# Kernel optimization log

Hardware: AMD Instinct MI355X
Metric: run time of the kernel (lower is better)

The kernel has to match this reference:

```python
import jax, jax.numpy as jnp
import numpy as np

D_MODEL = 2048
N_HEADS = 16
HEAD_DIM = D_MODEL // N_HEADS  # 128
BASE = 10000.0
NEG = -1e9


def _rope_tables(seq_len, dtype=jnp.float32):
    # inv_freq over even dims of head_dim, emb = cat(freqs, freqs)
    inv_freq = 1.0 / (BASE ** (jnp.arange(0, HEAD_DIM, 2, dtype=jnp.float32) / HEAD_DIM))
    t = jnp.arange(seq_len, dtype=jnp.float32)
    freqs = jnp.einsum('i,j->ij', t, inv_freq)          # [S, hd/2]
    emb = jnp.concatenate([freqs, freqs], axis=-1)       # [S, hd]
    return jnp.cos(emb).astype(dtype)[None, None], jnp.sin(emb).astype(dtype)[None, None]


def _rotate_half(x):
    # Faithful to source: rotary_ndims == head_dim, so x2 is empty and this returns x.
    x1, x2 = x[..., :HEAD_DIM], x[..., HEAD_DIM:]
    return jnp.concatenate([-x2, x1], axis=-1)


def setup_inputs() -> dict:
    key = jax.random.key(0)
    ks = jax.random.split(key, 5)
    B, S = 2, 2048
    x = jax.random.normal(ks[0], (B, S, D_MODEL), dtype=jnp.float32)
    # additive causal mask [1,1,S,S]
    causal = jnp.tril(jnp.ones((S, S), dtype=bool))
    attention_mask = jnp.where(causal, 0.0, NEG).astype(jnp.float32)[None, None]
    scale = 1.0 / np.sqrt(D_MODEL)
    Wq = jax.random.normal(ks[1], (D_MODEL, D_MODEL), dtype=jnp.float32) * scale
    Wk = jax.random.normal(ks[2], (D_MODEL, D_MODEL), dtype=jnp.float32) * scale
    Wv = jax.random.normal(ks[3], (D_MODEL, D_MODEL), dtype=jnp.float32) * scale
    Wd = jax.random.normal(ks[4], (D_MODEL, D_MODEL), dtype=jnp.float32) * scale
    return {"x": x, "attention_mask": attention_mask, "Wq": Wq, "Wk": Wk, "Wv": Wv, "Wd": Wd}


def reference(x, attention_mask, Wq, Wk, Wv, Wd):
    B, S, _ = x.shape
    # torch Linear: y = x @ W.T  (weights stored [out, in])
    def proj(W):
        y = jnp.einsum('bsd,ed->bse', x, W)
        return y.reshape(B, S, N_HEADS, HEAD_DIM).transpose(0, 2, 1, 3)  # [B,H,S,hd]
    q, k, v = proj(Wq), proj(Wk), proj(Wv)
    cos, sin = _rope_tables(S, x.dtype)
    q = q * cos + _rotate_half(q) * sin
    k = k * cos + _rotate_half(k) * sin
    scores = jnp.einsum('bhqd,bhkd->bhqk', q, k) / jnp.sqrt(jnp.float32(HEAD_DIM)).astype(x.dtype)
    scores = scores + attention_mask
    attn = jax.nn.softmax(scores, axis=-1)
    out = jnp.einsum('bhqk,bhkd->bhqd', attn, v)
    out = out.transpose(0, 2, 1, 3).reshape(B, S, D_MODEL)
    return jnp.einsum('bse,de->bsd', out, Wd)
```

## Files before the change

kernel.cpp:

```cpp
#include <hip/hip_runtime.h>
#include <stdint.h>

#define DM   2048
#define NH   16
#define HD   128
#define BB   2
#define SS   2048
#define MM   (BB*SS)
#define KK   2048
#define NQKV (3*DM)

#define LOG2E  1.4426950408889634f
#define SCALE  0.08838834764831845f

using bf16x8 = __attribute__((ext_vector_type(8))) __bf16;
using f32x4  = __attribute__((ext_vector_type(4))) float;
typedef unsigned short u16;
typedef unsigned int   u32;

__device__ __forceinline__ u16 f2bf(float f) {
  u32 u = __float_as_uint(f);
  u32 r = (u + 0x7FFFu + ((u >> 16) & 1u)) >> 16;
  return (u16)r;
}

__device__ __forceinline__ void load_lds16(const void* g, void* l) {
  __builtin_amdgcn_global_load_lds(
      (__attribute__((address_space(1))) void*)(g),
      (__attribute__((address_space(3))) void*)(l), 16, 0, 0);
}

__global__ void cast_f32_bf16(const float* __restrict__ s, u16* __restrict__ d, int n) {
  int i = (blockIdx.x * blockDim.x + threadIdx.x) * 4;
  if (i < n) {
    float4 f = *(const float4*)(s + i);
    u32 lo = (u32)f2bf(f.x) | ((u32)f2bf(f.y) << 16);
    u32 hi = (u32)f2bf(f.z) | ((u32)f2bf(f.w) << 16);
    *(uint2*)(d + i) = make_uint2(lo, hi);
  }
}

__global__ void rope_fct(float* __restrict__ f) {
  int i = blockIdx.x * blockDim.x + threadIdx.x;
  if (i < SS * 128) {
    int s = i >> 7, j = i & 127;
    double inv = pow(10000.0, -(double)(j & 63) / 64.0);
    float ang = (float)s * (float)inv;
    float sn, cs;
    sincosf(ang, &sn, &cs);
    f[i] = cs + sn;
  }
}

__global__ __launch_bounds__(256, 2)
void gemm_qkv_rope(const u16* __restrict__ A, const u16* __restrict__ Bm,
                   u16* __restrict__ qo, u16* __restrict__ ko, u16* __restrict__ vo,
                   const float* __restrict__ fct) {
  __shared__ __align__(16) u16 S[2][128 * 32];
  u16* As = S[0];
  u16* Bs = S[1];
  const int tid = threadIdx.x;
  const int w = tid >> 6, lane = tid & 63, ln = lane & 15, quad = lane >> 4;
  const int m0 = blockIdx.x * 128, n0 = blockIdx.y * 128;

  const f32x4 fz = {0.f, 0.f, 0.f, 0.f};
  f32x4 acc[2][8];
#pragma unroll
  for (int mt = 0; mt < 2; mt++)
#pragma unroll
    for (int nt = 0; nt < 8; nt++) acc[mt][nt] = fz;

  for (int k0 = 0; k0 < KK; k0 += 32) {
    __syncthreads();
#pragma unroll
    for (int i = 0; i < 2; i++) {
      int tt = i * 256 + tid;
      load_lds16(A + (size_t)(m0 + (tt >> 2)) * KK + k0 + (tt & 3) * 8, (char*)As + tt * 16);
    }
#pragma unroll
    for (int i = 0; i < 2; i++) {
      int tt = i * 256 + tid;
      load_lds16(Bm + (size_t)(n0 + (tt >> 2)) * KK + k0 + (tt & 3) * 8, (char*)Bs + tt * 16);
    }
    __syncthreads();
    bf16x8 af[2];
#pragma unroll
    for (int mt = 0; mt < 2; mt++)
      af[mt] = *(const bf16x8*)&As[(w * 32 + mt * 16 + ln) * 32 + quad * 8];
#pragma unroll
    for (int nt = 0; nt < 8; nt++) {
      bf16x8 bf = *(const bf16x8*)&Bs[(nt * 16 + ln) * 32 + quad * 8];
#pragma unroll
      for (int mt = 0; mt < 2; mt++)
        acc[mt][nt] = __builtin_amdgcn_mfma_f32_16x16x32_bf16(af[mt], bf, acc[mt][nt], 0, 0, 0);
    }
  }

  const int tensor = n0 >> 11;
  const int h = (n0 & 2047) >> 7;
  if (tensor < 2) {
    u16* dst = (tensor == 0) ? qo : ko;
#pragma unroll
    for (int mt = 0; mt < 2; mt++)
#pragma unroll
      for (int r = 0; r < 4; r++) {
        int m = m0 + w * 32 + mt * 16 + quad * 4 + r;
        int b = m >> 11, s = m & 2047;
        size_t base = ((size_t)(b * NH + h) * SS + s) * HD;
        const float* fr = fct + s * 128;
#pragma unroll
        for (int nt = 0; nt < 8; nt++) {
          int j = nt * 16 + ln;
          dst[base + j] = f2bf(acc[mt][nt][r] * fr[j]);
        }
      }
  } else {
    u16* Tr = (u16*)S;
    const int b = m0 >> 11, s0 = m0 & 2047;
#pragma unroll
    for (int mt = 0; mt < 2; mt++) {
      __syncthreads();
#pragma unroll
      for (int nt = 0; nt < 8; nt++) {
        int hd = nt * 16 + ln;
#pragma unroll
        for (int r = 0; r < 4; r++) {
          int c = w * 16 + quad * 4 + r;
          Tr[hd * 64 + (((c >> 3) ^ (hd & 7)) * 8) + (c & 7)] = f2bf(acc[mt][nt][r]);
        }
      }
      __syncthreads();
#pragma unroll
      for (int it = 0; it < 4; it++) {
        int idx = it * 256 + tid;
        int hd = idx >> 3, c8 = idx & 7;
        uint4 val = *(const uint4*)&Tr[hd * 64 + ((c8 ^ (hd & 7)) * 8)];
        int c0 = c8 * 8;
        int srel = ((c0 >> 4) * 32) + mt * 16 + (c0 & 15);
        *(uint4*)(vo + ((size_t)(b * NH + h) * HD + hd) * SS + s0 + srel) = val;
      }
    }
  }
}

__global__ __launch_bounds__(256, 2)
void flash_attn(const u16* __restrict__ q, const u16* __restrict__ k,
                const u16* __restrict__ v, u16* __restrict__ o) {
  __shared__ __align__(16) u16 Ps[64 * 64];
  __shared__ __align__(16) u16 Ks[2][64 * 128];
  __shared__ __align__(16) u16 Vs[2][128 * 64];
  const int tid = threadIdx.x;
  const int w = tid >> 6, lane = tid & 63, ln = lane & 15, quad = lane >> 4;
  const int hh = blockIdx.y, b = blockIdx.z;
  const size_t bh = (size_t)b * NH + hh;
  const u16* Kg = k + bh * SS * HD;
  const u16* Vg = v + bh * HD * SS;

  for (int half = 0; half < 2; half++) {
    const int T = half ? (31 - (int)blockIdx.x) : (int)blockIdx.x;
    const u16* Qg = q + bh * SS * HD + (size_t)T * 64 * HD;

    bf16x8 qf[4];
#pragma unroll
    for (int kc = 0; kc < 4; kc++)
      qf[kc] = *(const bf16x8*)(Qg + (size_t)(w * 16 + ln) * HD + (kc * 4 + quad) * 8);

    __syncthreads();

#pragma unroll
    for (int i = 0; i < 4; i++) {
      int slot = i * 256 + tid;
      int r = slot >> 4, c = (slot & 15) ^ (r & 7);
      load_lds16(Kg + (size_t)r * HD + c * 8, (char*)Ks[0] + slot * 16);
    }
#pragma unroll
    for (int i = 0; i < 4; i++) {
      int slot = i * 256 + tid;
      int r = slot >> 3, c = (slot & 7) ^ (r & 7);
      load_lds16(Vg + (size_t)r * SS + c * 8, (char*)Vs[0] + slot * 16);
    }

    const f32x4 fz = {0.f, 0.f, 0.f, 0.f};
    float m_s[4], l_s[4];
    f32x4 accO[8];
#pragma unroll
    for (int r = 0; r < 4; r++) { m_s[r] = -1e30f; l_s[r] = 0.f; }
#pragma unroll
    for (int nt = 0; nt < 8; nt++) accO[nt] = fz;

    const int nkt = T + 1;
    const int qrb = T * 64 + w * 16;

    for (int kt = 0; kt < nkt; kt++) {
      const int cur = kt & 1;
      const int k0 = kt * 64;
      __asm__ __volatile__("s_waitcnt vmcnt(0)" ::: "memory");
      __syncthreads();
      if (kt + 1 < nkt) {
        const int kn = k0 + 64;
#pragma unroll
        for (int i = 0; i < 4; i++) {
          int slot = i * 256 + tid;
          int r = slot >> 4, c = (slot & 15) ^ (r & 7);
          load_lds16(Kg + (size_t)(kn + r) * HD + c * 8, (char*)Ks[cur ^ 1] + slot * 16);
        }
#pragma unroll
        for (int i = 0; i < 4; i++) {
          int slot = i * 256 + tid;
          int r = slot >> 3, c = (slot & 7) ^ (r & 7);
          load_lds16(Vg + (size_t)r * SS + kn + c * 8, (char*)Vs[cur ^ 1] + slot * 16);
        }
      }

      f32x4 sc[4];
#pragma unroll
      for (int nt = 0; nt < 4; nt++) sc[nt] = fz;
#pragma unroll
      for (int kc = 0; kc < 4; kc++)
#pragma unroll
        for (int nt = 0; nt < 4; nt++) {
          bf16x8 bf = *(const bf16x8*)&Ks[cur][(nt * 16 + ln) * 128 + (((kc * 4 + quad) ^ (ln & 7)) * 8)];
          sc[nt] = __builtin_amdgcn_mfma_f32_16x16x32_bf16(qf[kc], bf, sc[nt], 0, 0, 0);
        }

      const bool partial = (kt == T);
#pragma unroll
      for (int nt = 0; nt < 4; nt++)
#pragma unroll
        for (int r = 0; r < 4; r++) {
          float val = sc[nt][r] * SCALE;
          if (partial && (k0 + nt * 16 + ln > qrb + quad * 4 + r)) val = -1e9f;
          sc[nt][r] = val;
        }

#pragma unroll
      for (int r = 0; r < 4; r++) {
        float mx = fmaxf(fmaxf(sc[0][r], sc[1][r]), fmaxf(sc[2][r], sc[3][r]));
#pragma unroll
        for (int off = 1; off < 16; off <<= 1) mx = fmaxf(mx, __shfl_xor(mx, off));
        float mnew = fmaxf(m_s[r], mx);
        float alpha = exp2f((m_s[r] - mnew) * LOG2E);
        float rs = 0.f;
#pragma unroll
        for (int nt = 0; nt < 4; nt++) {
          float p = exp2f((sc[nt][r] - mnew) * LOG2E);
          sc[nt][r] = p;
          rs += p;
        }
#pragma unroll
        for (int off = 1; off < 16; off <<= 1) rs += __shfl_xor(rs, off);
        l_s[r] = l_s[r] * alpha + rs;
        m_s[r] = mnew;
#pragma unroll
        for (int nt = 0; nt < 8; nt++) accO[nt][r] *= alpha;
      }

#pragma unroll
      for (int nt = 0; nt < 4; nt++)
#pragma unroll
        for (int r = 0; r < 4; r++) {
          int rr = w * 16 + quad * 4 + r;
          int j = nt * 16 + ln;
          Ps[rr * 64 + (((j >> 3) ^ (rr & 7)) * 8) + (j & 7)] = f2bf(sc[nt][r]);
        }
      __asm__ __volatile__("s_waitcnt lgkmcnt(0)" ::: "memory");

      bf16x8 pf[2];
#pragma unroll
      for (int kc = 0; kc < 2; kc++) {
        int rp = w * 16 + ln;
        pf[kc] = *(const bf16x8*)&Ps[rp * 64 + (((kc * 4 + quad) ^ (ln & 7)) * 8)];
      }

#pragma unroll
      for (int kc = 0; kc < 2; kc++)
#pragma unroll
        for (int nt = 0; nt < 8; nt++) {
          bf16x8 vf = *(const bf16x8*)&Vs[cur][(nt * 16 + ln) * 64 + (((kc * 4 + quad) ^ (ln & 7)) * 8)];
          accO[nt] = __builtin_amdgcn_mfma_f32_16x16x32_bf16(pf[kc], vf, accO[nt], 0, 0, 0);
        }
    }

#pragma unroll
    for (int r = 0; r < 4; r++) {
      float ilv = 1.f / l_s[r];
      int srow = T * 64 + w * 16 + quad * 4 + r;
      size_t base = ((size_t)b * SS + srow) * DM + hh * HD;
#pragma unroll
      for (int nt = 0; nt < 8; nt++)
        o[base + nt * 16 + ln] = f2bf(accO[nt][r] * ilv);
    }
  }
}

__global__ __launch_bounds__(256, 2)
void gemm_out(const u16* __restrict__ A, const u16* __restrict__ Bm,
              float* __restrict__ C) {
  __shared__ __align__(16) u16 As[128 * 32];
  __shared__ __align__(16) u16 Bs[128 * 32];
  const int tid = threadIdx.x;
  const int w = tid >> 6, lane = tid & 63, ln = lane & 15, quad = lane >> 4;
  const int m0 = blockIdx.x * 128, n0 = blockIdx.y * 128;

  const f32x4 fz = {0.f, 0.f, 0.f, 0.f};
  f32x4 acc[2][8];
#pragma unroll
  for (int mt = 0; mt < 2; mt++)
#pragma unroll
    for (int nt = 0; nt < 8; nt++) acc[mt][nt] = fz;

  for (int k0 = 0; k0 < KK; k0 += 32) {
    __syncthreads();
#pragma unroll
    for (int i = 0; i < 2; i++) {
      int tt = i * 256 + tid;
      load_lds16(A + (size_t)(m0 + (tt >> 2)) * KK + k0 + (tt & 3) * 8, (char*)As + tt * 16);
    }
#pragma unroll
    for (int i = 0; i < 2; i++) {
      int tt = i * 256 + tid;
      load_lds16(Bm + (size_t)(n0 + (tt >> 2)) * KK + k0 + (tt & 3) * 8, (char*)Bs + tt * 16);
    }
    __syncthreads();
    bf16x8 af[2];
#pragma unroll
    for (int mt = 0; mt < 2; mt++)
      af[mt] = *(const bf16x8*)&As[(w * 32 + mt * 16 + ln) * 32 + quad * 8];
#pragma unroll
    for (int nt = 0; nt < 8; nt++) {
      bf16x8 bf = *(const bf16x8*)&Bs[(nt * 16 + ln) * 32 + quad * 8];
#pragma unroll
      for (int mt = 0; mt < 2; mt++)
        acc[mt][nt] = __builtin_amdgcn_mfma_f32_16x16x32_bf16(af[mt], bf, acc[mt][nt], 0, 0, 0);
    }
  }

#pragma unroll
  for (int mt = 0; mt < 2; mt++)
#pragma unroll
    for (int r = 0; r < 4; r++) {
      int m = m0 + w * 32 + mt * 16 + quad * 4 + r;
#pragma unroll
      for (int nt = 0; nt < 8; nt++)
        C[(size_t)m * DM + n0 + nt * 16 + ln] = acc[mt][nt][r];
    }
}

extern "C" void kernel_launch(void* const* d_in, const int* in_sizes, int n_in,
                              void* d_out, int out_size, void* d_ws, size_t ws_size,
                              hipStream_t stream) {
  (void)in_sizes; (void)n_in; (void)out_size; (void)ws_size;
  const float* x  = (const float*)d_in[0];
  const float* Wq = (const float*)d_in[2];
  const float* Wk = (const float*)d_in[3];
  const float* Wv = (const float*)d_in[4];
  const float* Wd = (const float*)d_in[5];

  char* ws = (char*)d_ws;
  u16* xb   = (u16*)(ws);
  u16* aob  = xb;
  u16* wqkv = (u16*)(ws + 16777216ull);
  float* fct = (float*)(ws + 41943040ull);
  u16* wdb  = (u16*)(ws + 41943040ull);
  u16* qb   = (u16*)(ws + 50331648ull);
  u16* kb   = (u16*)(ws + 67108864ull);
  u16* vtb  = (u16*)(ws + 83886080ull);

  cast_f32_bf16<<<8192, 256, 0, stream>>>(x,  xb, MM * KK);
  cast_f32_bf16<<<4096, 256, 0, stream>>>(Wq, wqkv,                   DM * KK);
  cast_f32_bf16<<<4096, 256, 0, stream>>>(Wk, wqkv + (size_t)DM*KK,   DM * KK);
  cast_f32_bf16<<<4096, 256, 0, stream>>>(Wv, wqkv + (size_t)2*DM*KK, DM * KK);
  rope_fct<<<1024, 256, 0, stream>>>(fct);

  gemm_qkv_rope<<<dim3(MM / 128, NQKV / 128), 256, 0, stream>>>(xb, wqkv, qb, kb, vtb, fct);

  cast_f32_bf16<<<4096, 256, 0, stream>>>(Wd, wdb, DM * KK);

  flash_attn<<<dim3(16, NH, BB), 256, 0, stream>>>(qb, kb, vtb, aob);
  gemm_out<<<dim3(MM / 128, DM / 128), 256, 0, stream>>>(aob, wdb, (float*)d_out);
}
```

Measured before the change: 423.2 us.

## Rewrite QKV GEMM with 256x256 tiles, double-buffered LDS and interleaved async loads

The QKV projection GEMM moves from 128x128 tiles with 256 threads and a synchronous k-step of 32 to 256x256 tiles with 512 threads and a k-step of 64. It uses XOR-swizzled, double-buffered LDS and stages the next tile in quarters between MFMA phases, with manual waitcnt, barrier and setprio control. The goal is more data reuse per load and hiding global-load latency behind MFMA work. In exchange it uses 128KB of LDS and a large accumulator set, which likely limits occupancy to one block per CU despite the launch bounds, and the V transpose epilogue is rewritten to match.

```diff
diff --git a/kernel.cpp b/kernel.cpp
--- a/kernel.cpp
+++ b/kernel.cpp
@@ -52,93 +52,195 @@
   }
 }
 
-__global__ __launch_bounds__(256, 2)
+
+__device__ __forceinline__ void stage_half(const u16* __restrict__ G, int rowbase,
+                                           int kbase, int h, u16* lds, int tid) {
+#pragma unroll
+  for (int i = 0; i < 2; i++) {
+    int s = i * 512 + tid;
+    int r = s >> 3, c = s & 7;
+    load_lds16(G + (size_t)(rowbase + h * 128 + r) * KK + kbase + ((c ^ (r & 7)) * 8),
+               (char*)lds + (size_t)(h * 1024 + s) * 16);
+  }
+}
+
+__global__ __launch_bounds__(512, 2)
 void gemm_qkv_rope(const u16* __restrict__ A, const u16* __restrict__ Bm,
                    u16* __restrict__ qo, u16* __restrict__ ko, u16* __restrict__ vo,
                    const float* __restrict__ fct) {
-  __shared__ __align__(16) u16 S[2][128 * 32];
-  u16* As = S[0];
-  u16* Bs = S[1];
+  __shared__ __align__(16) u16 L[2][2][256 * 64];
   const int tid = threadIdx.x;
-  const int w = tid >> 6, lane = tid & 63, ln = lane & 15, quad = lane >> 4;
-  const int m0 = blockIdx.x * 128, n0 = blockIdx.y * 128;
+  const int wid = tid >> 6, lane = tid & 63, ln = lane & 15, quad = lane >> 4;
+  const int wm = wid >> 2, wn = wid & 3;
+  const int m0 = blockIdx.x * 256, n0 = blockIdx.y * 256;
 
   const f32x4 fz = {0.f, 0.f, 0.f, 0.f};
-  f32x4 acc[2][8];
-#pragma unroll
-  for (int mt = 0; mt < 2; mt++)
-#pragma unroll
-    for (int nt = 0; nt < 8; nt++) acc[mt][nt] = fz;
-
-  for (int k0 = 0; k0 < KK; k0 += 32) {
-    __syncthreads();
-#pragma unroll
-    for (int i = 0; i < 2; i++) {
-      int tt = i * 256 + tid;
-      load_lds16(A + (size_t)(m0 + (tt >> 2)) * KK + k0 + (tt & 3) * 8, (char*)As + tt * 16);
-    }
-#pragma unroll
-    for (int i = 0; i < 2; i++) {
-      int tt = i * 256 + tid;
-      load_lds16(Bm + (size_t)(n0 + (tt >> 2)) * KK + k0 + (tt & 3) * 8, (char*)Bs + tt * 16);
-    }
-    __syncthreads();
-    bf16x8 af[2];
-#pragma unroll
-    for (int mt = 0; mt < 2; mt++)
-      af[mt] = *(const bf16x8*)&As[(w * 32 + mt * 16 + ln) * 32 + quad * 8];
-#pragma unroll
-    for (int nt = 0; nt < 8; nt++) {
-      bf16x8 bf = *(const bf16x8*)&Bs[(nt * 16 + ln) * 32 + quad * 8];
-#pragma unroll
-      for (int mt = 0; mt < 2; mt++)
-        acc[mt][nt] = __builtin_amdgcn_mfma_f32_16x16x32_bf16(af[mt], bf, acc[mt][nt], 0, 0, 0);
-    }
+  f32x4 acc[8][4];
+#pragma unroll
+  for (int mi = 0; mi < 8; mi++)
+#pragma unroll
+    for (int ni = 0; ni < 4; ni++) acc[mi][ni] = fz;
+
+  int aRow[8], bRow[4];
+#pragma unroll
+  for (int mi = 0; mi < 8; mi++)
+    aRow[mi] = ((mi < 4) ? (wm * 64 + mi * 16) : (128 + wm * 64 + (mi - 4) * 16)) + ln;
+#pragma unroll
+  for (int ni = 0; ni < 4; ni++)
+    bRow[ni] = ((ni < 2) ? (wn * 32 + ni * 16) : (128 + wn * 32 + (ni - 2) * 16)) + ln;
+
+  stage_half(A,  m0, 0, 0, L[0][0], tid);
+  stage_half(Bm, n0, 0, 0, L[0][1], tid);
+  stage_half(A,  m0, 0, 1, L[0][0], tid);
+  stage_half(Bm, n0, 0, 1, L[0][1], tid);
+
+  const int nT = KK / 64;
+  for (int t = 0; t < nT; t++) {
+    const int cur = t & 1;
+    const u16* At = L[cur][0];
+    const u16* Bt = L[cur][1];
+    u16* Ax = L[cur ^ 1][0];
+    u16* Bx = L[cur ^ 1][1];
+    const int kn = (t + 1) * 64;
+    const bool nl = (t + 1 < nT);
+    bf16x8 aF[2][4], bF0[2][2], bF1[2][2];
+
+    if (nl) { __asm__ __volatile__("s_waitcnt vmcnt(4)" ::: "memory"); }
+    else    { __asm__ __volatile__("s_waitcnt vmcnt(0)" ::: "memory"); }
+    __asm__ __volatile__("s_barrier" ::: "memory");
+#pragma unroll
+    for (int kk = 0; kk < 2; kk++) {
+#pragma unroll
+      for (int mi = 0; mi < 4; mi++)
+        aF[kk][mi] = *(const bf16x8*)&At[aRow[mi] * 64 + (((kk * 4 + quad) ^ (aRow[mi] & 7)) * 8)];
+#pragma unroll
+      for (int ni = 0; ni < 2; ni++)
+        bF0[kk][ni] = *(const bf16x8*)&Bt[bRow[ni] * 64 + (((kk * 4 + quad) ^ (bRow[ni] & 7)) * 8)];
+    }
+    if (nl) stage_half(A, m0, kn, 0, Ax, tid);
+    __asm__ __volatile__("s_waitcnt lgkmcnt(0)" ::: "memory");
+    __builtin_amdgcn_sched_barrier(0);
+    __builtin_amdgcn_s_setprio(1);
+#pragma unroll
+    for (int kk = 0; kk < 2; kk++)
+#pragma unroll
+      for (int mi = 0; mi < 4; mi++)
+#pragma unroll
+        for (int ni = 0; ni < 2; ni++)
+          acc[mi][ni] = __builtin_amdgcn_mfma_f32_16x16x32_bf16(aF[kk][mi], bF0[kk][ni], acc[mi][ni], 0, 0, 0);
+    __builtin_amdgcn_s_setprio(0);
+    __builtin_amdgcn_sched_barrier(0);
+
+    if (nl) { __asm__ __volatile__("s_waitcnt vmcnt(4)" ::: "memory"); }
+    __asm__ __volatile__("s_barrier" ::: "memory");
+#pragma unroll
+    for (int kk = 0; kk < 2; kk++)
+#pragma unroll
+      for (int mi = 0; mi < 4; mi++)
+        aF[kk][mi] = *(const bf16x8*)&At[aRow[4 + mi] * 64 + (((kk * 4 + quad) ^ (aRow[4 + mi] & 7)) * 8)];
+    if (nl) stage_half(Bm, n0, kn, 0, Bx, tid);
+    __asm__ __volatile__("s_waitcnt lgkmcnt(0)" ::: "memory");
+    __builtin_amdgcn_sched_barrier(0);
+    __builtin_amdgcn_s_setprio(1);
+#pragma unroll
+    for (int kk = 0; kk < 2; kk++)
+#pragma unroll
+      for (int mi = 0; mi < 4; mi++)
+#pragma unroll
+        for (int ni = 0; ni < 2; ni++)
+          acc[4 + mi][ni] = __builtin_amdgcn_mfma_f32_16x16x32_bf16(aF[kk][mi], bF0[kk][ni], acc[4 + mi][ni], 0, 0, 0);
+    __builtin_amdgcn_s_setprio(0);
+    __builtin_amdgcn_sched_barrier(0);
+
+    if (nl) { __asm__ __volatile__("s_waitcnt vmcnt(4)" ::: "memory"); }
+    __asm__ __volatile__("s_barrier" ::: "memory");
+#pragma unroll
+    for (int kk = 0; kk < 2; kk++)
+#pragma unroll
+      for (int ni = 0; ni < 2; ni++)
+        bF1[kk][ni] = *(const bf16x8*)&Bt[bRow[2 + ni] * 64 + (((kk * 4 + quad) ^ (bRow[2 + ni] & 7)) * 8)];
+    if (nl) stage_half(A, m0, kn, 1, Ax, tid);
+    __asm__ __volatile__("s_waitcnt lgkmcnt(0)" ::: "memory");
+    __builtin_amdgcn_sched_barrier(0);
+    __builtin_amdgcn_s_setprio(1);
+#pragma unroll
+    for (int kk = 0; kk < 2; kk++)
+#pragma unroll
+      for (int mi = 0; mi < 4; mi++)
+#pragma unroll
+        for (int ni = 0; ni < 2; ni++)
+          acc[4 + mi][2 + ni] = __builtin_amdgcn_mfma_f32_16x16x32_bf16(aF[kk][mi], bF1[kk][ni], acc[4 + mi][2 + ni], 0, 0, 0);
+    __builtin_amdgcn_s_setprio(0);
+    __builtin_amdgcn_sched_barrier(0);
+
+#pragma unroll
+    for (int kk = 0; kk < 2; kk++)
+#pragma unroll
+      for (int mi = 0; mi < 4; mi++)
+        aF[kk][mi] = *(const bf16x8*)&At[aRow[mi] * 64 + (((kk * 4 + quad) ^ (aRow[mi] & 7)) * 8)];
+    if (nl) stage_half(Bm, n0, kn, 1, Bx, tid);
+    __asm__ __volatile__("s_waitcnt lgkmcnt(0)" ::: "memory");
+    __builtin_amdgcn_sched_barrier(0);
+    __builtin_amdgcn_s_setprio(1);
+#pragma unroll
+    for (int kk = 0; kk < 2; kk++)
+#pragma unroll
+      for (int mi = 0; mi < 4; mi++)
+#pragma unroll
+        for (int ni = 0; ni < 2; ni++)
+          acc[mi][2 + ni] = __builtin_amdgcn_mfma_f32_16x16x32_bf16(aF[kk][mi], bF1[kk][ni], acc[mi][2 + ni], 0, 0, 0);
+    __builtin_amdgcn_s_setprio(0);
+    __builtin_amdgcn_sched_barrier(0);
   }
 
   const int tensor = n0 >> 11;
-  const int h = (n0 & 2047) >> 7;
+  const int nloc0 = n0 & 2047;
   if (tensor < 2) {
     u16* dst = (tensor == 0) ? qo : ko;
 #pragma unroll
-    for (int mt = 0; mt < 2; mt++)
+    for (int mi = 0; mi < 8; mi++) {
+      int rowM = (mi < 4) ? (wm * 64 + mi * 16) : (128 + wm * 64 + (mi - 4) * 16);
 #pragma unroll
       for (int r = 0; r < 4; r++) {
-        int m = m0 + w * 32 + mt * 16 + quad * 4 + r;
+        int m = m0 + rowM + quad * 4 + r;
         int b = m >> 11, s = m & 2047;
-        size_t base = ((size_t)(b * NH + h) * SS + s) * HD;
         const float* fr = fct + s * 128;
 #pragma unroll
-        for (int nt = 0; nt < 8; nt++) {
-          int j = nt * 16 + ln;
-          dst[base + j] = f2bf(acc[mt][nt][r] * fr[j]);
+        for (int ni = 0; ni < 4; ni++) {
+          int colN = ((ni < 2) ? (wn * 32 + ni * 16) : (128 + wn * 32 + (ni - 2) * 16)) + ln;
+          int h = (nloc0 + colN) >> 7;
+          int j = colN & 127;
+          dst[((size_t)(b * NH + h) * SS + s) * HD + j] = f2bf(acc[mi][ni][r] * fr[j]);
         }
       }
+    }
   } else {
-    u16* Tr = (u16*)S;
+    __syncthreads();
+    u16* Tr = (u16*)L;
     const int b = m0 >> 11, s0 = m0 & 2047;
 #pragma unroll
-    for (int mt = 0; mt < 2; mt++) {
-      __syncthreads();
-#pragma unroll
-      for (int nt = 0; nt < 8; nt++) {
-        int hd = nt * 16 + ln;
+    for (int mi = 0; mi < 8; mi++) {
+      int rowM = (mi < 4) ? (wm * 64 + mi * 16) : (128 + wm * 64 + (mi - 4) * 16);
+#pragma unroll
+      for (int ni = 0; ni < 4; ni++) {
+        int colN = ((ni < 2) ? (wn * 32 + ni * 16) : (128 + wn * 32 + (ni - 2) * 16)) + ln;
 #pragma unroll
         for (int r = 0; r < 4; r++) {
-          int c = w * 16 + quad * 4 + r;
-          Tr[hd * 64 + (((c >> 3) ^ (hd & 7)) * 8) + (c & 7)] = f2bf(acc[mt][nt][r]);
+          int srel = rowM + quad * 4 + r;
+          int ch = srel >> 3;
+          Tr[colN * 256 + ((ch ^ (colN & 31)) * 8) + (srel & 7)] = f2bf(acc[mi][ni][r]);
         }
       }
-      __syncthreads();
-#pragma unroll
-      for (int it = 0; it < 4; it++) {
-        int idx = it * 256 + tid;
-        int hd = idx >> 3, c8 = idx & 7;
-        uint4 val = *(const uint4*)&Tr[hd * 64 + ((c8 ^ (hd & 7)) * 8)];
-        int c0 = c8 * 8;
-        int srel = ((c0 >> 4) * 32) + mt * 16 + (c0 & 15);
-        *(uint4*)(vo + ((size_t)(b * NH + h) * HD + hd) * SS + s0 + srel) = val;
-      }
+    }
+    __syncthreads();
+#pragma unroll
+    for (int it = 0; it < 16; it++) {
+      int slot = it * 512 + tid;
+      int nloc = slot >> 5, c8 = slot & 31;
+      uint4 val = *(const uint4*)&Tr[nloc * 256 + ((c8 ^ (nloc & 31)) * 8)];
+      int h = (nloc0 >> 7) + (nloc >> 7);
+      int hd = nloc & 127;
+      *(uint4*)(vo + ((size_t)(b * NH + h) * HD + hd) * SS + s0 + c8 * 8) = val;
     }
   }
 }
@@ -372,7 +474,7 @@
   cast_f32_bf16<<<4096, 256, 0, stream>>>(Wv, wqkv + (size_t)2*DM*KK, DM * KK);
   rope_fct<<<1024, 256, 0, stream>>>(fct);
 
-  gemm_qkv_rope<<<dim3(MM / 128, NQKV / 128), 256, 0, stream>>>(xb, wqkv, qb, kb, vtb, fct);
+  gemm_qkv_rope<<<dim3(MM / 256, NQKV / 256), 512, 0, stream>>>(xb, wqkv, qb, kb, vtb, fct);
 
   cast_f32_bf16<<<4096, 256, 0, stream>>>(Wd, wdb, DM * KK);
 
```

Result: faster. 409.0 us (-3.4%).

## Rewrite QKV and output GEMMs with double-buffered swizzled LDS and larger tiles

Applied to the files above, without the earlier changes.

Both projection GEMMs now share one main loop that uses 256x128 tiles with 512 threads, BK=64, and double-buffered LDS. Global-to-LDS loads for the next tile are issued while MFMAs run on the current one, using manual waitcnt/barrier and setprio scheduling. LDS rows are XOR-swizzled to avoid bank conflicts. The V transpose epilogue is redone for the larger tile. The intent is to hide global memory latency and remove the two full syncthreads per 32-wide k-step, at the cost of about 96KB of LDS per block, which limits occupancy, and fragile hand-written wait counts.

```diff
diff --git a/kernel.cpp b/kernel.cpp
--- a/kernel.cpp
+++ b/kernel.cpp
@@ -52,93 +52,166 @@
   }
 }
 
-__global__ __launch_bounds__(256, 2)
+
+__device__ __forceinline__ void stage_unit(const u16* __restrict__ G, int rowbase,
+                                           int kbase, u16* lds, int tid) {
+#pragma unroll
+  for (int i = 0; i < 2; i++) {
+    int s = i * 512 + tid;
+    int r = s >> 3, c = s & 7;
+    load_lds16(G + (size_t)(rowbase + r) * KK + kbase + ((c ^ (r & 7)) * 8),
+               (char*)lds + (size_t)s * 16);
+  }
+}
+
+#define GEMM_MAIN_LOOP(EXTRA_LAST)                                              \
+  const int tid = threadIdx.x;                                                  \
+  const int wid = tid >> 6, lane = tid & 63, ln = lane & 15, quad = lane >> 4;  \
+  const int wm = wid >> 2, wn = wid & 3;                                        \
+  const int m0 = blockIdx.x * 256, n0 = blockIdx.y * 128;                       \
+  const f32x4 fz = {0.f, 0.f, 0.f, 0.f};                                        \
+  f32x4 acc[8][2];                                                              \
+  _Pragma("unroll") for (int mi = 0; mi < 8; mi++)                              \
+    _Pragma("unroll") for (int ni = 0; ni < 2; ni++) acc[mi][ni] = fz;          \
+  int aRow[8], bRow[2];                                                         \
+  _Pragma("unroll") for (int mi = 0; mi < 8; mi++)                              \
+    aRow[mi] = ((mi < 4) ? (wm * 64 + mi * 16)                                  \
+                         : (128 + wm * 64 + (mi - 4) * 16)) + ln;               \
+  _Pragma("unroll") for (int ni = 0; ni < 2; ni++)                              \
+    bRow[ni] = wn * 32 + ni * 16 + ln;                                          \
+                        \
+  stage_unit(Bm, n0, 0, LB[0], tid);                                            \
+  stage_unit(A, m0, 0, LA[0], tid);                                             \
+  stage_unit(A, m0 + 128, 0, LA[0] + 128 * 64, tid);                            \
+  const int nT = KK / 64;                                                       \
+  for (int t = 0; t < nT; t++) {                                                \
+    const int cur = t & 1;                                                      \
+    const u16* At = LA[cur];                                                    \
+    const u16* Bt = LB[cur];                                                    \
+    u16* Ax = LA[cur ^ 1];                                                      \
+    u16* Bx = LB[cur ^ 1];                                                      \
+    const int kn = (t + 1) * 64;                                                \
+    const bool nl = (t + 1 < nT);                                               \
+    bf16x8 aF[2][4], bF[2][2];                                                  \
+                                    \
+    __asm__ __volatile__("s_waitcnt vmcnt(2)" ::: "memory");                    \
+    __asm__ __volatile__("s_barrier" ::: "memory");                             \
+    _Pragma("unroll") for (int kk = 0; kk < 2; kk++) {                          \
+      _Pragma("unroll") for (int mi = 0; mi < 4; mi++)                          \
+        aF[kk][mi] = *(const bf16x8*)&At[aRow[mi] * 64 +                        \
+                      (((kk * 4 + quad) ^ (aRow[mi] & 7)) * 8)];                \
+      _Pragma("unroll") for (int ni = 0; ni < 2; ni++)                          \
+        bF[kk][ni] = *(const bf16x8*)&Bt[bRow[ni] * 64 +                        \
+                      (((kk * 4 + quad) ^ (bRow[ni] & 7)) * 8)];                \
+    }                                                                           \
+    if (nl) stage_unit(Bm, n0, kn, Bx, tid);                                    \
+    __asm__ __volatile__("s_waitcnt lgkmcnt(0)" ::: "memory");                  \
+    __builtin_amdgcn_sched_barrier(0);                                          \
+    __builtin_amdgcn_s_setprio(1);                                              \
+    _Pragma("unroll") for (int kk = 0; kk < 2; kk++)                            \
+      _Pragma("unroll") for (int mi = 0; mi < 4; mi++)                          \
+        _Pragma("unroll") for (int ni = 0; ni < 2; ni++)                        \
+          acc[mi][ni] = __builtin_amdgcn_mfma_f32_16x16x32_bf16(                \
+              aF[kk][mi], bF[kk][ni], acc[mi][ni], 0, 0, 0);                    \
+    __builtin_amdgcn_s_setprio(0);                                              \
+    __builtin_amdgcn_sched_barrier(0);                                          \
+                                  \
+    if (nl) { __asm__ __volatile__("s_waitcnt vmcnt(2)" ::: "memory"); }        \
+    else    { __asm__ __volatile__("s_waitcnt vmcnt(0)" ::: "memory"); }        \
+    __asm__ __volatile__("s_barrier" ::: "memory");                             \
+    _Pragma("unroll") for (int kk = 0; kk < 2; kk++)                            \
+      _Pragma("unroll") for (int mi = 0; mi < 4; mi++)                          \
+        aF[kk][mi] = *(const bf16x8*)&At[aRow[4 + mi] * 64 +                    \
+                      (((kk * 4 + quad) ^ (aRow[4 + mi] & 7)) * 8)];            \
+    if (nl) {                                                                   \
+      stage_unit(A, m0, kn, Ax, tid);                                           \
+      stage_unit(A, m0 + 128, kn, Ax + 128 * 64, tid);                          \
+    }                                                                           \
+    __asm__ __volatile__("s_waitcnt lgkmcnt(0)" ::: "memory");                  \
+    __builtin_amdgcn_sched_barrier(0);                                          \
+    __builtin_amdgcn_s_setprio(1);                                              \
+    _Pragma("unroll") for (int kk = 0; kk < 2; kk++)                            \
+      _Pragma("unroll") for (int mi = 0; mi < 4; mi++)                          \
+        _Pragma("unroll") for (int ni = 0; ni < 2; ni++)                        \
+          acc[4 + mi][ni] = __builtin_amdgcn_mfma_f32_16x16x32_bf16(            \
+              aF[kk][mi], bF[kk][ni], acc[4 + mi][ni], 0, 0, 0);                \
+    __builtin_amdgcn_s_setprio(0);                                              \
+    __builtin_amdgcn_sched_barrier(0);                                          \
+    (void)0; EXTRA_LAST                                                         \
+  }
+
+__global__ __launch_bounds__(512, 2)
 void gemm_qkv_rope(const u16* __restrict__ A, const u16* __restrict__ Bm,
                    u16* __restrict__ qo, u16* __restrict__ ko, u16* __restrict__ vo,
                    const float* __restrict__ fct) {
-  __shared__ __align__(16) u16 S[2][128 * 32];
-  u16* As = S[0];
-  u16* Bs = S[1];
-  const int tid = threadIdx.x;
-  const int w = tid >> 6, lane = tid & 63, ln = lane & 15, quad = lane >> 4;
-  const int m0 = blockIdx.x * 128, n0 = blockIdx.y * 128;
-
-  const f32x4 fz = {0.f, 0.f, 0.f, 0.f};
-  f32x4 acc[2][8];
-#pragma unroll
-  for (int mt = 0; mt < 2; mt++)
-#pragma unroll
-    for (int nt = 0; nt < 8; nt++) acc[mt][nt] = fz;
-
-  for (int k0 = 0; k0 < KK; k0 += 32) {
-    __syncthreads();
-#pragma unroll
-    for (int i = 0; i < 2; i++) {
-      int tt = i * 256 + tid;
-      load_lds16(A + (size_t)(m0 + (tt >> 2)) * KK + k0 + (tt & 3) * 8, (char*)As + tt * 16);
-    }
-#pragma unroll
-    for (int i = 0; i < 2; i++) {
-      int tt = i * 256 + tid;
-      load_lds16(Bm + (size_t)(n0 + (tt >> 2)) * KK + k0 + (tt & 3) * 8, (char*)Bs + tt * 16);
-    }
-    __syncthreads();
-    bf16x8 af[2];
-#pragma unroll
-    for (int mt = 0; mt < 2; mt++)
-      af[mt] = *(const bf16x8*)&As[(w * 32 + mt * 16 + ln) * 32 + quad * 8];
-#pragma unroll
-    for (int nt = 0; nt < 8; nt++) {
-      bf16x8 bf = *(const bf16x8*)&Bs[(nt * 16 + ln) * 32 + quad * 8];
-#pragma unroll
-      for (int mt = 0; mt < 2; mt++)
-        acc[mt][nt] = __builtin_amdgcn_mfma_f32_16x16x32_bf16(af[mt], bf, acc[mt][nt], 0, 0, 0);
-    }
-  }
+  __shared__ __align__(16) u16 LA[2][256 * 64];
+  __shared__ __align__(16) u16 LB[2][128 * 64];
+  GEMM_MAIN_LOOP()
 
   const int tensor = n0 >> 11;
   const int h = (n0 & 2047) >> 7;
   if (tensor < 2) {
     u16* dst = (tensor == 0) ? qo : ko;
 #pragma unroll
-    for (int mt = 0; mt < 2; mt++)
+    for (int mi = 0; mi < 8; mi++) {
+      int rowM = (mi < 4) ? (wm * 64 + mi * 16) : (128 + wm * 64 + (mi - 4) * 16);
 #pragma unroll
       for (int r = 0; r < 4; r++) {
-        int m = m0 + w * 32 + mt * 16 + quad * 4 + r;
+        int m = m0 + rowM + quad * 4 + r;
         int b = m >> 11, s = m & 2047;
-        size_t base = ((size_t)(b * NH + h) * SS + s) * HD;
         const float* fr = fct + s * 128;
 #pragma unroll
-        for (int nt = 0; nt < 8; nt++) {
-          int j = nt * 16 + ln;
-          dst[base + j] = f2bf(acc[mt][nt][r] * fr[j]);
+        for (int ni = 0; ni < 2; ni++) {
+          int j = wn * 32 + ni * 16 + ln;
+          dst[((size_t)(b * NH + h) * SS + s) * HD + j] = f2bf(acc[mi][ni][r] * fr[j]);
         }
       }
+    }
   } else {
-    u16* Tr = (u16*)S;
+    __syncthreads();
+    u16* Tr = (u16*)LA;
     const int b = m0 >> 11, s0 = m0 & 2047;
 #pragma unroll
-    for (int mt = 0; mt < 2; mt++) {
-      __syncthreads();
-#pragma unroll
-      for (int nt = 0; nt < 8; nt++) {
-        int hd = nt * 16 + ln;
+    for (int mi = 0; mi < 8; mi++) {
+      int rowM = (mi < 4) ? (wm * 64 + mi * 16) : (128 + wm * 64 + (mi - 4) * 16);
+#pragma unroll
+      for (int ni = 0; ni < 2; ni++) {
+        int hd = wn * 32 + ni * 16 + ln;
 #pragma unroll
         for (int r = 0; r < 4; r++) {
-          int c = w * 16 + quad * 4 + r;
-          Tr[hd * 64 + (((c >> 3) ^ (hd & 7)) * 8) + (c & 7)] = f2bf(acc[mt][nt][r]);
+          int srel = rowM + quad * 4 + r;
+          int ch = srel >> 3;
+          Tr[hd * 256 + ((ch ^ (hd & 31)) * 8) + (srel & 7)] = f2bf(acc[mi][ni][r]);
         }
       }
-      __syncthreads();
-#pragma unroll
-      for (int it = 0; it < 4; it++) {
-        int idx = it * 256 + tid;
-        int hd = idx >> 3, c8 = idx & 7;
-        uint4 val = *(const uint4*)&Tr[hd * 64 + ((c8 ^ (hd & 7)) * 8)];
-        int c0 = c8 * 8;
-        int srel = ((c0 >> 4) * 32) + mt * 16 + (c0 & 15);
-        *(uint4*)(vo + ((size_t)(b * NH + h) * HD + hd) * SS + s0 + srel) = val;
-      }
+    }
+    __syncthreads();
+#pragma unroll
+    for (int it = 0; it < 8; it++) {
+      int slot = it * 512 + tid;
+      int hd = slot >> 5, c8 = slot & 31;
+      uint4 val = *(const uint4*)&Tr[hd * 256 + ((c8 ^ (hd & 31)) * 8)];
+      *(uint4*)(vo + ((size_t)(b * NH + h) * HD + hd) * SS + s0 + c8 * 8) = val;
+    }
+  }
+}
+
+__global__ __launch_bounds__(512, 2)
+void gemm_out(const u16* __restrict__ A, const u16* __restrict__ Bm,
+              float* __restrict__ C) {
+  __shared__ __align__(16) u16 LA[2][256 * 64];
+  __shared__ __align__(16) u16 LB[2][128 * 64];
+  GEMM_MAIN_LOOP()
+
+#pragma unroll
+  for (int mi = 0; mi < 8; mi++) {
+    int rowM = (mi < 4) ? (wm * 64 + mi * 16) : (128 + wm * 64 + (mi - 4) * 16);
+#pragma unroll
+    for (int r = 0; r < 4; r++) {
+      int m = m0 + rowM + quad * 4 + r;
+#pragma unroll
+      for (int ni = 0; ni < 2; ni++)
+        C[(size_t)m * DM + n0 + wn * 32 + ni * 16 + ln] = acc[mi][ni][r];
     }
   }
 }
@@ -293,59 +366,6 @@
   }
 }
 
-__global__ __launch_bounds__(256, 2)
-void gemm_out(const u16* __restrict__ A, const u16* __restrict__ Bm,
-              float* __restrict__ C) {
-  __shared__ __align__(16) u16 As[128 * 32];
-  __shared__ __align__(16) u16 Bs[128 * 32];
-  const int tid = threadIdx.x;
-  const int w = tid >> 6, lane = tid & 63, ln = lane & 15, quad = lane >> 4;
-  const int m0 = blockIdx.x * 128, n0 = blockIdx.y * 128;
-
-  const f32x4 fz = {0.f, 0.f, 0.f, 0.f};
-  f32x4 acc[2][8];
-#pragma unroll
-  for (int mt = 0; mt < 2; mt++)
-#pragma unroll
-    for (int nt = 0; nt < 8; nt++) acc[mt][nt] = fz;
-
-  for (int k0 = 0; k0 < KK; k0 += 32) {
-    __syncthreads();
-#pragma unroll
-    for (int i = 0; i < 2; i++) {
-      int tt = i * 256 + tid;
-      load_lds16(A + (size_t)(m0 + (tt >> 2)) * KK + k0 + (tt & 3) * 8, (char*)As + tt * 16);
-    }
-#pragma unroll
-    for (int i = 0; i < 2; i++) {
-      int tt = i * 256 + tid;
-      load_lds16(Bm + (size_t)(n0 + (tt >> 2)) * KK + k0 + (tt & 3) * 8, (char*)Bs + tt * 16);
-    }
-    __syncthreads();
-    bf16x8 af[2];
-#pragma unroll
-    for (int mt = 0; mt < 2; mt++)
-      af[mt] = *(const bf16x8*)&As[(w * 32 + mt * 16 + ln) * 32 + quad * 8];
-#pragma unroll
-    for (int nt = 0; nt < 8; nt++) {
-      bf16x8 bf = *(const bf16x8*)&Bs[(nt * 16 + ln) * 32 + quad * 8];
-#pragma unroll
-      for (int mt = 0; mt < 2; mt++)
-        acc[mt][nt] = __builtin_amdgcn_mfma_f32_16x16x32_bf16(af[mt], bf, acc[mt][nt], 0, 0, 0);
-    }
-  }
-
-#pragma unroll
-  for (int mt = 0; mt < 2; mt++)
-#pragma unroll
-    for (int r = 0; r < 4; r++) {
-      int m = m0 + w * 32 + mt * 16 + quad * 4 + r;
-#pragma unroll
-      for (int nt = 0; nt < 8; nt++)
-        C[(size_t)m * DM + n0 + nt * 16 + ln] = acc[mt][nt][r];
-    }
-}
-
 extern "C" void kernel_launch(void* const* d_in, const int* in_sizes, int n_in,
                               void* d_out, int out_size, void* d_ws, size_t ws_size,
                               hipStream_t stream) {
@@ -372,10 +392,10 @@
   cast_f32_bf16<<<4096, 256, 0, stream>>>(Wv, wqkv + (size_t)2*DM*KK, DM * KK);
   rope_fct<<<1024, 256, 0, stream>>>(fct);
 
-  gemm_qkv_rope<<<dim3(MM / 128, NQKV / 128), 256, 0, stream>>>(xb, wqkv, qb, kb, vtb, fct);
+  gemm_qkv_rope<<<dim3(MM / 256, NQKV / 128), 512, 0, stream>>>(xb, wqkv, qb, kb, vtb, fct);
 
   cast_f32_bf16<<<4096, 256, 0, stream>>>(Wd, wdb, DM * KK);
 
   flash_attn<<<dim3(16, NH, BB), 256, 0, stream>>>(qb, kb, vtb, aob);
-  gemm_out<<<dim3(MM / 128, DM / 128), 256, 0, stream>>>(aob, wdb, (float*)d_out);
-}
+  gemm_out<<<dim3(MM / 256, DM / 128), 512, 0, stream>>>(aob, wdb, (float*)d_out);
+}
```

Measured after the change: 400.9 us. 1.06x faster.
